# Kernel tuning notes

Hardware: AMD Instinct MI355X
Metric: run time of the kernel (lower is better)

## Reference

```python
import jax, jax.numpy as jnp
import numpy as np

N = 50000      # nodes
E = 800000     # edges
IN = 128       # in_feats
HID = 16       # h_feats (per head)
HEADS = 8      # num_heads layer 1
CLS = 40       # num_classes
NEG_SLOPE = 0.2


def setup_inputs() -> dict:
    key = jax.random.key(0)
    ks = jax.random.split(key, 12)
    s = lambda fan: np.float32(1.0 / np.sqrt(fan))
    return {
        "features": jax.random.normal(ks[0], (N, IN), jnp.float32),
        "edge_src": jax.random.randint(ks[1], (E,), 0, N, dtype=jnp.int32),
        "edge_dst": jax.random.randint(ks[2], (E,), 0, N, dtype=jnp.int32),
        # layer 1 params
        "W1": jax.random.normal(ks[3], (IN, HEADS * HID), jnp.float32) * s(IN),
        "al1": jax.random.normal(ks[4], (HEADS, HID), jnp.float32) * s(HID),
        "ar1": jax.random.normal(ks[5], (HEADS, HID), jnp.float32) * s(HID),
        "b1": jnp.zeros((HEADS * HID,), jnp.float32),
        # layer 2 params (1 head)
        "W2": jax.random.normal(ks[6], (HEADS * HID, CLS), jnp.float32) * s(HEADS * HID),
        "al2": jax.random.normal(ks[7], (1, CLS), jnp.float32) * s(CLS),
        "ar2": jax.random.normal(ks[8], (1, CLS), jnp.float32) * s(CLS),
        "b2": jnp.zeros((CLS,), jnp.float32),
    }


def gat_conv(x, W, al, ar, b, src, dst, heads, out_dim):
    # x: [N, F_in] -> feat: [N, H, D]
    feat = (x @ W).reshape(-1, heads, out_dim)
    el = (feat * al).sum(-1)                      # [N, H]
    er = (feat * ar).sum(-1)                      # [N, H]
    e = jax.nn.leaky_relu(el[src] + er[dst], NEG_SLOPE)  # [E, H]
    # segment softmax over destination neighborhoods
    emax = jax.ops.segment_max(e, dst, num_segments=N)   # [N, H]
    emax = jnp.where(jnp.isfinite(emax), emax, jnp.float32(0.0))
    ee = jnp.exp(e - emax[dst])                   # [E, H]
    denom = jax.ops.segment_sum(ee, dst, num_segments=N)
    alpha = ee / (denom[dst] + jnp.float32(1e-9)) # [E, H]
    msg = alpha[:, :, None] * feat[src]           # [E, H, D]
    out = jax.ops.segment_sum(msg, dst, num_segments=N)  # [N, H, D]
    return out + b.reshape(1, heads, out_dim)


def reference(features, edge_src, edge_dst, W1, al1, ar1, b1, W2, al2, ar2, b2):
    h = jax.nn.elu(gat_conv(features, W1, al1, ar1, b1, edge_src, edge_dst, HEADS, HID))
    h = h.reshape(N, HEADS * HID)                 # flatten(1)
    out = gat_conv(h, W2, al2, ar2, b2, edge_src, edge_dst, 1, CLS)
    return out.mean(axis=1)                       # [N, CLS]
```

## Files before the change

### kernel.cpp

```cpp
#include <hip/hip_runtime.h>
#include <hip/hip_bf16.h>

#define N_NODES 50000
#define N_EDGES 800000
#define IN_F    128
#define HID     16
#define HEADS   8
#define F1      128
#define CLS     40
#define CLSP    64
#define NEG     0.2f
#define NEG_INF (-__builtin_inff())
#define SWEEPS      8
#define SWEEP_RANGE 6250
#define STRIDE      96

typedef __bf16 bf16x8 __attribute__((ext_vector_type(8)));
typedef float  f32x4  __attribute__((ext_vector_type(4)));
typedef float  f32x2  __attribute__((ext_vector_type(2)));

__device__ __forceinline__ float leaky(float v) { return v >= 0.0f ? v : NEG * v; }
__device__ __forceinline__ f32x2 unpk(unsigned u) {
    f32x2 r;
    r.x = __uint_as_float(u << 16);
    r.y = __uint_as_float(u & 0xffff0000u);
    return r;
}

__global__ void setup_kernel(const float* __restrict__ W1, const float* __restrict__ W2,
                             __bf16* __restrict__ w1t, __bf16* __restrict__ w2t,
                             int* __restrict__ cursor) {
    int i = blockIdx.x * blockDim.x + threadIdx.x;
    if (i < N_NODES) cursor[i] = 0;
    if (i < 128 * 128) {
        int n = i >> 7, k = i & 127;
        w1t[i] = (__bf16)W1[k * 128 + n];
    }
    if (i < CLSP * 128) {
        int n = i >> 7, k = i & 127;
        w2t[i] = (n < CLS) ? (__bf16)W2[k * CLS + n] : (__bf16)0.0f;
    }
}

__global__ void scatter_kernel(const int* __restrict__ src, const int* __restrict__ dst,
                               int* __restrict__ cursor, int* __restrict__ srcs_sorted) {
    const int BPS = (N_EDGES + 255) / 256;
    int sweep = blockIdx.x / BPS;
    int e = (blockIdx.x - sweep * BPS) * 256 + threadIdx.x;
    if (e >= N_EDGES) return;
    int d = dst[e];
    int lo = sweep * SWEEP_RANGE;
    if (d < lo || d >= lo + SWEEP_RANGE) return;
    int pos = d * STRIDE + atomicAdd(&cursor[d], 1);
    srcs_sorted[pos] = src[e];
}

__global__ __launch_bounds__(256) void gemm1_mfma(const float* __restrict__ A,
                                                  const __bf16* __restrict__ Wt,
                                                  const float* __restrict__ al1,
                                                  const float* __restrict__ ar1,
                                                  __bf16* __restrict__ outb,
                                                  float* __restrict__ el,
                                                  float* __restrict__ er) {
    int wave = threadIdx.x >> 6, lane = threadIdx.x & 63;
    int m0 = blockIdx.x * 64 + wave * 16;
    int c = lane & 15;
    int row = m0 + c;
    int rowc = row < N_NODES ? row : N_NODES - 1;
    int ko = (lane >> 4) * 8;

    f32x4 acc[8];
    #pragma unroll
    for (int t = 0; t < 8; ++t)
        #pragma unroll
        for (int r = 0; r < 4; ++r) acc[t][r] = 0.f;

    for (int ks = 0; ks < 128; ks += 32) {
        const float* ap = A + (size_t)rowc * 128 + ks + ko;
        float4 u = *(const float4*)ap;
        float4 v = *(const float4*)(ap + 4);
        bf16x8 a;
        a[0] = (__bf16)u.x; a[1] = (__bf16)u.y; a[2] = (__bf16)u.z; a[3] = (__bf16)u.w;
        a[4] = (__bf16)v.x; a[5] = (__bf16)v.y; a[6] = (__bf16)v.z; a[7] = (__bf16)v.w;
        #pragma unroll
        for (int t = 0; t < 8; ++t) {
            bf16x8 b = *(const bf16x8*)(Wt + (size_t)(t * 16 + c) * 128 + ks + ko);
            acc[t] = __builtin_amdgcn_mfma_f32_16x16x32_bf16(a, b, acc[t], 0, 0, 0);
        }
    }
    int rbase = m0 + (lane >> 4) * 4;
    #pragma unroll
    for (int t = 0; t < 8; ++t) {
        int gcol = t * 16 + c;
        #pragma unroll
        for (int r = 0; r < 4; ++r) {
            int grow = rbase + r;
            if (grow < N_NODES) outb[(size_t)grow * 128 + gcol] = (__bf16)acc[t][r];
        }
    }
    #pragma unroll
    for (int t = 0; t < 8; ++t) {
        float alv = al1[t * 16 + c];
        float arv = ar1[t * 16 + c];
        float pe[4], pr[4];
        #pragma unroll
        for (int r = 0; r < 4; ++r) { pe[r] = acc[t][r] * alv; pr[r] = acc[t][r] * arv; }
        #pragma unroll
        for (int mask = 1; mask <= 8; mask <<= 1) {
            #pragma unroll
            for (int r = 0; r < 4; ++r) {
                pe[r] += __shfl_xor(pe[r], mask, 64);
                pr[r] += __shfl_xor(pr[r], mask, 64);
            }
        }
        if (c == 0) {
            #pragma unroll
            for (int r = 0; r < 4; ++r) {
                int grow = rbase + r;
                if (grow < N_NODES) {
                    el[grow * 8 + t] = pe[r];
                    er[grow * 8 + t] = pr[r];
                }
            }
        }
    }
}

__global__ __launch_bounds__(256) void gemm2_mfma(const __bf16* __restrict__ A,
                                                  const __bf16* __restrict__ Wt,
                                                  const float* __restrict__ al2,
                                                  const float* __restrict__ ar2,
                                                  __bf16* __restrict__ out,
                                                  float* __restrict__ el,
                                                  float* __restrict__ er) {
    int wave = threadIdx.x >> 6, lane = threadIdx.x & 63;
    int m0 = blockIdx.x * 64 + wave * 16;
    int c = lane & 15;
    int row = m0 + c;
    int rowc = row < N_NODES ? row : N_NODES - 1;
    int ko = (lane >> 4) * 8;

    f32x4 acc[4];
    #pragma unroll
    for (int t = 0; t < 4; ++t)
        #pragma unroll
        for (int r = 0; r < 4; ++r) acc[t][r] = 0.f;

    for (int ks = 0; ks < 128; ks += 32) {
        bf16x8 a = *(const bf16x8*)(A + (size_t)rowc * 128 + ks + ko);
        #pragma unroll
        for (int t = 0; t < 4; ++t) {
            bf16x8 b = *(const bf16x8*)(Wt + (size_t)(t * 16 + c) * 128 + ks + ko);
            acc[t] = __builtin_amdgcn_mfma_f32_16x16x32_bf16(a, b, acc[t], 0, 0, 0);
        }
    }
    int rbase = m0 + (lane >> 4) * 4;
    #pragma unroll
    for (int t = 0; t < 4; ++t) {
        int gcol = t * 16 + c;
        #pragma unroll
        for (int r = 0; r < 4; ++r) {
            int grow = rbase + r;
            if (grow < N_NODES) out[(size_t)grow * CLSP + gcol] = (__bf16)acc[t][r];
        }
    }
    float pe[4] = {0.f, 0.f, 0.f, 0.f}, pr[4] = {0.f, 0.f, 0.f, 0.f};
    #pragma unroll
    for (int t = 0; t < 3; ++t) {
        int idx = t * 16 + c;
        float alv = (idx < CLS) ? al2[idx] : 0.f;
        float arv = (idx < CLS) ? ar2[idx] : 0.f;
        #pragma unroll
        for (int r = 0; r < 4; ++r) { pe[r] += acc[t][r] * alv; pr[r] += acc[t][r] * arv; }
    }
    #pragma unroll
    for (int mask = 1; mask <= 8; mask <<= 1) {
        #pragma unroll
        for (int r = 0; r < 4; ++r) {
            pe[r] += __shfl_xor(pe[r], mask, 64);
            pr[r] += __shfl_xor(pr[r], mask, 64);
        }
    }
    if (c == 0) {
        #pragma unroll
        for (int r = 0; r < 4; ++r) {
            int grow = rbase + r;
            if (grow < N_NODES) { el[grow] = pe[r]; er[grow] = pr[r]; }
        }
    }
}

__global__ __launch_bounds__(256) void gat1_fused(const int* __restrict__ degs,
                                                  const int* __restrict__ srcs,
                                                  const float* __restrict__ el,
                                                  const float* __restrict__ er,
                                                  const __bf16* __restrict__ feat1b,
                                                  const float* __restrict__ b1,
                                                  __bf16* __restrict__ hbufb) {
    __shared__ float a_lds[4][32 * 8];
    int wave = threadIdx.x >> 6;
    int lane = threadIdx.x & 63;
    int d = blockIdx.x * 4 + wave;
    int off = d * STRIDE;
    int deg = degs[d];

    int h = lane & 7, slot = lane >> 3;
    int q = lane >> 4, fg = lane & 15, hd = fg >> 1;
    float er_d = er[d * 8 + h];

    f32x2 accv[4];
    #pragma unroll
    for (int j = 0; j < 4; ++j) { accv[j].x = 0.f; accv[j].y = 0.f; }

    bool fast = (deg <= 32);
    uint4 p[8];
    if (fast) {
        #pragma unroll
        for (int g = 0; g < 8; ++g) {
            int k = g * 4 + q;
            if (k < deg) {
                int se = srcs[off + k];
                p[g] = *(const uint4*)(feat1b + (size_t)se * F1 + fg * 8);
            }
        }
        float sc[4];
        float m = NEG_INF;
        #pragma unroll
        for (int it = 0; it < 4; ++it) {
            float v = NEG_INF;
            int e = it * 8 + slot;
            if (e < deg) {
                int s = srcs[off + e];
                v = leaky(el[s * 8 + h] + er_d);
            }
            sc[it] = v;
            m = fmaxf(m, v);
        }
        float l = 0.f;
        #pragma unroll
        for (int it = 0; it < 4; ++it)
            l += (sc[it] == NEG_INF) ? 0.f : __expf(sc[it] - m);
        #pragma unroll
        for (int mask = 8; mask <= 32; mask <<= 1) {
            float m2 = __shfl_xor(m, mask, 64);
            float l2 = __shfl_xor(l, mask, 64);
            float mn = fmaxf(m, m2);
            float f1 = (m  == NEG_INF) ? 0.f : __expf(m - mn);
            float f2 = (m2 == NEG_INF) ? 0.f : __expf(m2 - mn);
            l = l * f1 + l2 * f2;
            m = mn;
        }
        float inv_l = 1.f / (l + 1e-9f);
        #pragma unroll
        for (int it = 0; it < 4; ++it) {
            int e = it * 8 + slot;
            if (e < deg)
                a_lds[wave][e * 8 + h] = __expf(sc[it] - m) * inv_l;
        }
    }
    __syncthreads();

    if (fast) {
        #pragma unroll
        for (int g = 0; g < 8; ++g) {
            int k = g * 4 + q;
            if (k < deg) {
                float a = a_lds[wave][k * 8 + hd];
                f32x2 av; av.x = a; av.y = a;
                accv[0] += av * unpk(p[g].x);
                accv[1] += av * unpk(p[g].y);
                accv[2] += av * unpk(p[g].z);
                accv[3] += av * unpk(p[g].w);
            }
        }
    } else {
        float m = NEG_INF, l = 0.f;
        for (int base = 0; base < deg; base += 8) {
            int e = base + slot;
            float v = NEG_INF;
            if (e < deg) {
                int s = srcs[off + e];
                v = leaky(el[s * 8 + h] + er_d);
            }
            float mn = fmaxf(m, v);
            float f1 = (m == NEG_INF) ? 0.f : __expf(m - mn);
            float f2 = (v == NEG_INF) ? 0.f : __expf(v - mn);
            l = l * f1 + f2;
            m = mn;
        }
        #pragma unroll
        for (int mask = 8; mask <= 32; mask <<= 1) {
            float m2 = __shfl_xor(m, mask, 64);
            float l2 = __shfl_xor(l, mask, 64);
            float mn = fmaxf(m, m2);
            float f1 = (m  == NEG_INF) ? 0.f : __expf(m - mn);
            float f2 = (m2 == NEG_INF) ? 0.f : __expf(m2 - mn);
            l = l * f1 + l2 * f2;
            m = mn;
        }
        float inv_l = 1.f / (l + 1e-9f);

        for (int base = 0; base < deg; base += 8) {
            int e = base + slot;
            float alpha = 0.f;
            int s = 0;
            if (e < deg) {
                s = srcs[off + e];
                float v = leaky(el[s * 8 + h] + er_d);
                alpha = __expf(v - m) * inv_l;
            }
            #pragma unroll
            for (int sub = 0; sub < 2; ++sub) {
                int k = sub * 4 + q;
                float a  = __shfl(alpha, k * 8 + hd, 64);
                int   se = __shfl(s,     k * 8,      64);
                uint4 pp = *(const uint4*)(feat1b + (size_t)se * F1 + fg * 8);
                f32x2 av; av.x = a; av.y = a;
                accv[0] += av * unpk(pp.x);
                accv[1] += av * unpk(pp.y);
                accv[2] += av * unpk(pp.z);
                accv[3] += av * unpk(pp.w);
            }
        }
    }

    float acc[8];
    #pragma unroll
    for (int j = 0; j < 4; ++j) { acc[2 * j] = accv[j].x; acc[2 * j + 1] = accv[j].y; }
    #pragma unroll
    for (int i = 0; i < 8; ++i) {
        acc[i] += __shfl_xor(acc[i], 16, 64);
        acc[i] += __shfl_xor(acc[i], 32, 64);
    }
    if (q == 0) {
        bf16x8 o;
        #pragma unroll
        for (int i = 0; i < 8; ++i) {
            float v = acc[i] + b1[fg * 8 + i];
            v = v > 0.f ? v : expm1f(v);
            o[i] = (__bf16)v;
        }
        *(bf16x8*)(hbufb + (size_t)d * F1 + fg * 8) = o;
    }
}

__global__ __launch_bounds__(256) void gat2_fused(const int* __restrict__ degs,
                                                  const int* __restrict__ srcs,
                                                  const float* __restrict__ el,
                                                  const float* __restrict__ er,
                                                  const __bf16* __restrict__ feat2p,
                                                  const float* __restrict__ b2,
                                                  float* __restrict__ out) {
    __shared__ float a_lds[4][32];
    int wave = threadIdx.x >> 6;
    int lane = threadIdx.x & 63;
    int d = blockIdx.x * 4 + wave;
    int off = d * STRIDE;
    int deg = degs[d];

    float er_d = er[d];
    int q  = lane >> 4;
    int cg = lane & 15;
    f32x2 accv[2];
    accv[0].x = 0.f; accv[0].y = 0.f; accv[1].x = 0.f; accv[1].y = 0.f;

    bool fast = (deg <= 32);
    uint2 p[8];
    if (fast) {
        #pragma unroll
        for (int g = 0; g < 8; ++g) {
            int k = g * 4 + q;
            if (k < deg) {
                int se = srcs[off + k];
                p[g] = *(const uint2*)(feat2p + (size_t)se * CLSP + cg * 4);
            }
        }
        float sc = NEG_INF;
        if (lane < deg) {
            int s0 = srcs[off + lane];
            sc = leaky(el[s0] + er_d);
        }
        float m = sc, l = (sc == NEG_INF) ? 0.f : 1.f;
        #pragma unroll
        for (int mask = 1; mask <= 32; mask <<= 1) {
            float m2 = __shfl_xor(m, mask, 64);
            float l2 = __shfl_xor(l, mask, 64);
            float mn = fmaxf(m, m2);
            float f1 = (m  == NEG_INF) ? 0.f : __expf(m - mn);
            float f2 = (m2 == NEG_INF) ? 0.f : __expf(m2 - mn);
            l = l * f1 + l2 * f2;
            m = mn;
        }
        float inv_l = 1.f / (l + 1e-9f);
        if (lane < deg)
            a_lds[wave][lane] = __expf(sc - m) * inv_l;
    }
    __syncthreads();

    if (fast) {
        #pragma unroll
        for (int g = 0; g < 8; ++g) {
            int k = g * 4 + q;
            if (k < deg) {
                float a = a_lds[wave][k];
                f32x2 av; av.x = a; av.y = a;
                accv[0] += av * unpk(p[g].x);
                accv[1] += av * unpk(p[g].y);
            }
        }
    } else {
        float m = NEG_INF, l = 0.f;
        for (int base = 0; base < deg; base += 64) {
            int e = base + lane;
            float sc = NEG_INF;
            if (e < deg) {
                int s = srcs[off + e];
                sc = leaky(el[s] + er_d);
            }
            float mn = fmaxf(m, sc);
            float f1 = (m  == NEG_INF) ? 0.f : __expf(m - mn);
            float f2 = (sc == NEG_INF) ? 0.f : __expf(sc - mn);
            l = l * f1 + f2;
            m = mn;
        }
        #pragma unroll
        for (int mask = 1; mask <= 32; mask <<= 1) {
            float m2 = __shfl_xor(m, mask, 64);
            float l2 = __shfl_xor(l, mask, 64);
            float mn = fmaxf(m, m2);
            float f1 = (m  == NEG_INF) ? 0.f : __expf(m - mn);
            float f2 = (m2 == NEG_INF) ? 0.f : __expf(m2 - mn);
            l = l * f1 + l2 * f2;
            m = mn;
        }
        float inv_l = 1.f / (l + 1e-9f);

        for (int base = 0; base < deg; base += 64) {
            int e = base + lane;
            float alpha = 0.f;
            int s = 0;
            if (e < deg) {
                s = srcs[off + e];
                float sc = leaky(el[s] + er_d);
                alpha = __expf(sc - m) * inv_l;
            }
            int kmax = min(64, deg - base);
            int nsub = (kmax + 3) >> 2;
            for (int sub = 0; sub < nsub; ++sub) {
                int k = sub * 4 + q;
                float a  = __shfl(alpha, k, 64);
                int   se = __shfl(s,     k, 64);
                uint2 pp = *(const uint2*)(feat2p + (size_t)se * CLSP + cg * 4);
                f32x2 av; av.x = a; av.y = a;
                accv[0] += av * unpk(pp.x);
                accv[1] += av * unpk(pp.y);
            }
        }
    }

    float acc[4];
    acc[0] = accv[0].x; acc[1] = accv[0].y; acc[2] = accv[1].x; acc[3] = accv[1].y;
    #pragma unroll
    for (int i = 0; i < 4; ++i) {
        acc[i] += __shfl_xor(acc[i], 16, 64);
        acc[i] += __shfl_xor(acc[i], 32, 64);
    }
    if (lane < 10) {
        float4 o;
        o.x = acc[0] + b2[cg * 4 + 0];
        o.y = acc[1] + b2[cg * 4 + 1];
        o.z = acc[2] + b2[cg * 4 + 2];
        o.w = acc[3] + b2[cg * 4 + 3];
        *(float4*)(out + (size_t)d * CLS + cg * 4) = o;
    }
}

extern "C" void kernel_launch(void* const* d_in, const int* in_sizes, int n_in,
                              void* d_out, int out_size, void* d_ws, size_t ws_size,
                              hipStream_t stream) {
    const float* features = (const float*)d_in[0];
    const int*   esrc     = (const int*)d_in[1];
    const int*   edst     = (const int*)d_in[2];
    const float* W1       = (const float*)d_in[3];
    const float* al1      = (const float*)d_in[4];
    const float* ar1      = (const float*)d_in[5];
    const float* b1       = (const float*)d_in[6];
    const float* W2       = (const float*)d_in[7];
    const float* al2      = (const float*)d_in[8];
    const float* ar2      = (const float*)d_in[9];
    const float* b2       = (const float*)d_in[10];
    float* out = (float*)d_out;

    float* ws = (float*)d_ws;
    float*  el1    = ws;
    float*  er1    = ws + 400000;
    float*  el2    = ws + 800000;
    float*  er2    = ws + 850000;
    int*    cursor = (int*)(ws + 900000);
    int*    srcs   = (int*)(ws + 950000);
    __bf16* feat1b = (__bf16*)(ws + 5750000);
    __bf16* hbufb  = (__bf16*)(ws + 8950000);
    __bf16* feat2p = (__bf16*)(ws + 12150000);
    __bf16* w1t    = (__bf16*)(ws + 13750000);
    __bf16* w2t    = (__bf16*)(ws + 13760000);

    const int B = 256;
    const int BPS = (N_EDGES + 255) / 256;

    setup_kernel<<<(N_NODES + B - 1) / B, B, 0, stream>>>(W1, W2, w1t, w2t, cursor);
    scatter_kernel<<<SWEEPS * BPS, B, 0, stream>>>(esrc, edst, cursor, srcs);

    gemm1_mfma<<<(N_NODES + 63) / 64, 256, 0, stream>>>(features, w1t, al1, ar1,
                                                        feat1b, el1, er1);
    gat1_fused<<<N_NODES / 4, B, 0, stream>>>(cursor, srcs, el1, er1, feat1b, b1, hbufb);

    gemm2_mfma<<<(N_NODES + 63) / 64, 256, 0, stream>>>(hbufb, w2t, al2, ar2,
                                                        feat2p, el2, er2);
    gat2_fused<<<N_NODES / 4, B, 0, stream>>>(cursor, srcs, el2, er2, feat2p, b2, out);
}
```

Before: 276.9 us.

## Gather neighbor features in source-index sweeps after softmax instead of prefetching

In both GAT aggregation kernels the fast path no longer prefetches all neighbor feature rows before the softmax. It now stashes source indices in LDS and, after the barrier, gathers rows in four passes over source-id windows. The intent is to give the gather temporal locality, so concurrent waves touch similar node ranges and get more L2 hits. The cost is that the feature loads are no longer overlapped with the softmax computation, and each pass adds branching with more serialized load latency.

```diff
diff --git a/kernel.cpp b/kernel.cpp
--- a/kernel.cpp
+++ b/kernel.cpp
@@ -14,6 +14,8 @@
 #define SWEEPS      8
 #define SWEEP_RANGE 6250
 #define STRIDE      96
+#define GSWEEPS     4
+#define GWIN        12500
 
 typedef __bf16 bf16x8 __attribute__((ext_vector_type(8)));
 typedef float  f32x4  __attribute__((ext_vector_type(4)));
@@ -198,6 +200,7 @@
                                                   const float* __restrict__ b1,
                                                   __bf16* __restrict__ hbufb) {
     __shared__ float a_lds[4][32 * 8];
+    __shared__ int   s_lds[4][32];
     int wave = threadIdx.x >> 6;
     int lane = threadIdx.x & 63;
     int d = blockIdx.x * 4 + wave;
@@ -213,25 +216,17 @@
     for (int j = 0; j < 4; ++j) { accv[j].x = 0.f; accv[j].y = 0.f; }
 
     bool fast = (deg <= 32);
-    uint4 p[8];
     if (fast) {
-        #pragma unroll
-        for (int g = 0; g < 8; ++g) {
-            int k = g * 4 + q;
-            if (k < deg) {
-                int se = srcs[off + k];
-                p[g] = *(const uint4*)(feat1b + (size_t)se * F1 + fg * 8);
-            }
-        }
         float sc[4];
+        int sreg[4];
         float m = NEG_INF;
         #pragma unroll
         for (int it = 0; it < 4; ++it) {
             float v = NEG_INF;
             int e = it * 8 + slot;
             if (e < deg) {
-                int s = srcs[off + e];
-                v = leaky(el[s * 8 + h] + er_d);
+                sreg[it] = srcs[off + e];
+                v = leaky(el[sreg[it] * 8 + h] + er_d);
             }
             sc[it] = v;
             m = fmaxf(m, v);
@@ -254,23 +249,41 @@
         #pragma unroll
         for (int it = 0; it < 4; ++it) {
             int e = it * 8 + slot;
-            if (e < deg)
+            if (e < deg) {
                 a_lds[wave][e * 8 + h] = __expf(sc[it] - m) * inv_l;
+                if (h == 0) s_lds[wave][e] = sreg[it];
+            }
         }
     }
     __syncthreads();
 
     if (fast) {
+        int   se[8];
+        float av[8];
         #pragma unroll
         for (int g = 0; g < 8; ++g) {
             int k = g * 4 + q;
             if (k < deg) {
-                float a = a_lds[wave][k * 8 + hd];
-                f32x2 av; av.x = a; av.y = a;
-                accv[0] += av * unpk(p[g].x);
-                accv[1] += av * unpk(p[g].y);
-                accv[2] += av * unpk(p[g].z);
-                accv[3] += av * unpk(p[g].w);
+                se[g] = s_lds[wave][k];
+                av[g] = a_lds[wave][k * 8 + hd];
+            } else {
+                se[g] = -1;
+                av[g] = 0.f;
+            }
+        }
+        #pragma unroll
+        for (int s = 0; s < GSWEEPS; ++s) {
+            int lo = s * GWIN;
+            #pragma unroll
+            for (int g = 0; g < 8; ++g) {
+                if (se[g] >= lo && se[g] < lo + GWIN) {
+                    uint4 p = *(const uint4*)(feat1b + (size_t)se[g] * F1 + fg * 8);
+                    f32x2 a2; a2.x = av[g]; a2.y = av[g];
+                    accv[0] += a2 * unpk(p.x);
+                    accv[1] += a2 * unpk(p.y);
+                    accv[2] += a2 * unpk(p.z);
+                    accv[3] += a2 * unpk(p.w);
+                }
             }
         }
     } else {
@@ -313,13 +326,13 @@
             for (int sub = 0; sub < 2; ++sub) {
                 int k = sub * 4 + q;
                 float a  = __shfl(alpha, k * 8 + hd, 64);
-                int   se = __shfl(s,     k * 8,      64);
-                uint4 pp = *(const uint4*)(feat1b + (size_t)se * F1 + fg * 8);
-                f32x2 av; av.x = a; av.y = a;
-                accv[0] += av * unpk(pp.x);
-                accv[1] += av * unpk(pp.y);
-                accv[2] += av * unpk(pp.z);
-                accv[3] += av * unpk(pp.w);
+                int   ss = __shfl(s,     k * 8,      64);
+                uint4 pp = *(const uint4*)(feat1b + (size_t)ss * F1 + fg * 8);
+                f32x2 a2; a2.x = a; a2.y = a;
+                accv[0] += a2 * unpk(pp.x);
+                accv[1] += a2 * unpk(pp.y);
+                accv[2] += a2 * unpk(pp.z);
+                accv[3] += a2 * unpk(pp.w);
             }
         }
     }
@@ -352,6 +365,7 @@
                                                   const float* __restrict__ b2,
                                                   float* __restrict__ out) {
     __shared__ float a_lds[4][32];
+    __shared__ int   s_lds[4][32];
     int wave = threadIdx.x >> 6;
     int lane = threadIdx.x & 63;
     int d = blockIdx.x * 4 + wave;
@@ -365,19 +379,11 @@
     accv[0].x = 0.f; accv[0].y = 0.f; accv[1].x = 0.f; accv[1].y = 0.f;
 
     bool fast = (deg <= 32);
-    uint2 p[8];
     if (fast) {
-        #pragma unroll
-        for (int g = 0; g < 8; ++g) {
-            int k = g * 4 + q;
-            if (k < deg) {
-                int se = srcs[off + k];
-                p[g] = *(const uint2*)(feat2p + (size_t)se * CLSP + cg * 4);
-            }
-        }
         float sc = NEG_INF;
+        int s0 = 0;
         if (lane < deg) {
-            int s0 = srcs[off + lane];
+            s0 = srcs[off + lane];
             sc = leaky(el[s0] + er_d);
         }
         float m = sc, l = (sc == NEG_INF) ? 0.f : 1.f;
@@ -392,20 +398,38 @@
             m = mn;
         }
         float inv_l = 1.f / (l + 1e-9f);
-        if (lane < deg)
+        if (lane < deg) {
             a_lds[wave][lane] = __expf(sc - m) * inv_l;
+            s_lds[wave][lane] = s0;
+        }
     }
     __syncthreads();
 
     if (fast) {
+        int   se[8];
+        float av[8];
         #pragma unroll
         for (int g = 0; g < 8; ++g) {
             int k = g * 4 + q;
             if (k < deg) {
-                float a = a_lds[wave][k];
-                f32x2 av; av.x = a; av.y = a;
-                accv[0] += av * unpk(p[g].x);
-                accv[1] += av * unpk(p[g].y);
+                se[g] = s_lds[wave][k];
+                av[g] = a_lds[wave][k];
+            } else {
+                se[g] = -1;
+                av[g] = 0.f;
+            }
+        }
+        #pragma unroll
+        for (int s = 0; s < GSWEEPS; ++s) {
+            int lo = s * GWIN;
+            #pragma unroll
+            for (int g = 0; g < 8; ++g) {
+                if (se[g] >= lo && se[g] < lo + GWIN) {
+                    uint2 p = *(const uint2*)(feat2p + (size_t)se[g] * CLSP + cg * 4);
+                    f32x2 a2; a2.x = av[g]; a2.y = av[g];
+                    accv[0] += a2 * unpk(p.x);
+                    accv[1] += a2 * unpk(p.y);
+                }
             }
         }
     } else {
@@ -449,11 +473,11 @@
             for (int sub = 0; sub < nsub; ++sub) {
                 int k = sub * 4 + q;
                 float a  = __shfl(alpha, k, 64);
-                int   se = __shfl(s,     k, 64);
-                uint2 pp = *(const uint2*)(feat2p + (size_t)se * CLSP + cg * 4);
-                f32x2 av; av.x = a; av.y = a;
-                accv[0] += av * unpk(pp.x);
-                accv[1] += av * unpk(pp.y);
+                int   ss = __shfl(s,     k, 64);
+                uint2 pp = *(const uint2*)(feat2p + (size_t)ss * CLSP + cg * 4);
+                f32x2 a2; a2.x = a; a2.y = a;
+                accv[0] += a2 * unpk(pp.x);
+                accv[1] += a2 * unpk(pp.y);
             }
         }
     }
```

New measurement: 316.0 us. +14.1%, slower.
